# Performance work log

Measured on AMD Instinct MI355X. Metric: run time of the kernel, lower is better.

## Reference

```python
import jax, jax.numpy as jnp
import numpy as np

N, C, H, K, HID = 131072, 256, 8, 128, 1024
SCALE = (C // H) ** -0.5  # 1/sqrt(32)


def layernorm(x, g, b, eps=1e-5):
    mu = jnp.mean(x, axis=-1, keepdims=True)
    var = jnp.var(x, axis=-1, keepdims=True)
    return (x - mu) * jax.lax.rsqrt(var + eps) * g + b


def setup_inputs() -> dict:
    key = jax.random.key(0)
    ks = jax.random.split(key, 8)
    feat = jax.random.normal(ks[0], (N, C), dtype=jnp.float32)
    order = jax.random.permutation(ks[1], N)  # serialized order (gather)
    inverse = jnp.argsort(order)              # scatter back (unpad identity)
    s = 0.02
    return {
        "feat": feat,
        "ln1_g": jnp.ones((C,), jnp.float32), "ln1_b": jnp.zeros((C,), jnp.float32),
        "w_qkv": jax.random.normal(ks[2], (C, 3 * C), jnp.float32) * s,
        "b_qkv": jnp.zeros((3 * C,), jnp.float32),
        "w_proj": jax.random.normal(ks[3], (C, C), jnp.float32) * s,
        "b_proj": jnp.zeros((C,), jnp.float32),
        "ln2_g": jnp.ones((C,), jnp.float32), "ln2_b": jnp.zeros((C,), jnp.float32),
        "w1": jax.random.normal(ks[4], (C, HID), jnp.float32) * s,
        "b1": jnp.zeros((HID,), jnp.float32),
        "w2": jax.random.normal(ks[5], (HID, C), jnp.float32) * s,
        "b2": jnp.zeros((C,), jnp.float32),
        "order": order,
        "inverse": inverse,
    }


def attention(x, w_qkv, b_qkv, w_proj, b_proj, order, inverse):
    D = C // H
    qkv = x @ w_qkv + b_qkv                       # [N, 3C]
    qkv = qkv[order]                              # gather to serialized order
    qkv = qkv.reshape(-1, K, 3, H, D)             # [P, K, 3, H, D]
    q, k, v = jnp.moveaxis(qkv, 2, 0)             # each [P, K, H, D]
    q = jnp.swapaxes(q, 1, 2)                     # [P, H, K, D]
    k = jnp.swapaxes(k, 1, 2)
    v = jnp.swapaxes(v, 1, 2)
    attn = jnp.einsum("phkd,phjd->phkj", q * SCALE, k)  # [P, H, K, K]
    attn = jax.nn.softmax(attn, axis=-1)
    out = jnp.einsum("phkj,phjd->phkd", attn, v)  # [P, H, K, D]
    out = jnp.swapaxes(out, 1, 2).reshape(-1, C)  # [N, C]
    out = out[inverse]                            # scatter back to input order
    return out @ w_proj + b_proj


def reference(feat, ln1_g, ln1_b, w_qkv, b_qkv, w_proj, b_proj,
              ln2_g, ln2_b, w1, b1, w2, b2, order, inverse):
    # pre-norm transformer block: x + attn(ln1(x)); x + mlp(ln2(x))
    x = feat
    x = x + attention(layernorm(x, ln1_g, ln1_b), w_qkv, b_qkv, w_proj, b_proj, order, inverse)
    h = layernorm(x, ln2_g, ln2_b)
    h = jax.nn.gelu(h @ w1 + b1) @ w2 + b2
    return x + h
```

## Files before the change

kernel.cpp:

```cpp
#include <hip/hip_runtime.h>
#include <hip/hip_bf16.h>

typedef __hip_bfloat16 bf16;
typedef __bf16 bf16x8 __attribute__((ext_vector_type(8)));
typedef float f32x4 __attribute__((ext_vector_type(4)));

#define N_TOK 131072
#define C_DIM 256
#define HID_DIM 1024

__device__ __forceinline__ void async_copy16(void* lds, const void* g) {
  __builtin_amdgcn_global_load_lds(
      (const __attribute__((address_space(1))) void*)g,
      (__attribute__((address_space(3))) void*)lds, 16, 0, 0);
}

__device__ __forceinline__ float fast_rcp(float x) {
#if __has_builtin(__builtin_amdgcn_rcpf)
  return __builtin_amdgcn_rcpf(x);
#else
  return 1.f / x;
#endif
}

__device__ __forceinline__ bf16 bf16_rne(float f) {
  unsigned u = __float_as_uint(f);
  u += 0x7FFF + ((u >> 16) & 1);
  unsigned short s = (unsigned short)(u >> 16);
  return *reinterpret_cast<bf16*>(&s);
}

__device__ __forceinline__ float fast_gelu(float x) {
  float t = x * x;
  float u = __builtin_fmaf(0.07135481627f, t, 1.5957691216f);
  float z = x * u;
  float e = __expf(-z);
  return x * fast_rcp(1.f + e);
}

__global__ void ln_bf16_kernel(const float* __restrict__ x,
                               const float* __restrict__ g,
                               const float* __restrict__ b,
                               bf16* __restrict__ out) {
  int row = blockIdx.x * 4 + threadIdx.y;
  int lane = threadIdx.x;
  size_t base = (size_t)row * C_DIM + lane * 4;
  float4 v = *(const float4*)(x + base);
  float s = v.x + v.y + v.z + v.w;
  float s2 = v.x * v.x + v.y * v.y + v.z * v.z + v.w * v.w;
#pragma unroll
  for (int m = 1; m < 64; m <<= 1) { s += __shfl_xor(s, m); s2 += __shfl_xor(s2, m); }
  float mean = s * (1.f / 256.f);
  float var = s2 * (1.f / 256.f) - mean * mean;
  float rstd = rsqrtf(var + 1e-5f);
  float4 gv = *(const float4*)(g + lane * 4);
  float4 bv = *(const float4*)(b + lane * 4);
  union { bf16 h[4]; uint2 u; } pk;
  pk.h[0] = bf16_rne((v.x - mean) * rstd * gv.x + bv.x);
  pk.h[1] = bf16_rne((v.y - mean) * rstd * gv.y + bv.y);
  pk.h[2] = bf16_rne((v.z - mean) * rstd * gv.z + bv.z);
  pk.h[3] = bf16_rne((v.w - mean) * rstd * gv.w + bv.w);
  *(uint2*)(out + base) = pk.u;
}

__global__ void cast_transpose_kernel(const float* __restrict__ in, bf16* __restrict__ out,
                                      int K, int N) {
  int idx = blockIdx.x * 256 + threadIdx.x;
  if (idx >= K * N) return;
  int n = idx / K, k = idx - n * K;
  out[idx] = bf16_rne(in[(size_t)k * N + n]);
}

template <int EPI, int NXT>
__global__ __launch_bounds__(256) void gemm_bt_kernel(
    const bf16* __restrict__ A, const bf16* __restrict__ Bt,
    const float* __restrict__ bias, const float* __restrict__ res,
    void* __restrict__ outp, int K, int ldn) {
  __shared__ bf16 sA[128 * 64];
  __shared__ bf16 sB[128 * 64];
  const int bid = blockIdx.x;
  const int xcd = bid & 7;
  const int j = bid >> 3;
  const int n0 = (j % NXT) * 128;
  const int m0 = ((j / NXT) * 8 + xcd) * 128;
  const int tid = threadIdx.x;
  const int wid = tid >> 6;
  const int lane = tid & 63;
  const int quad = lane >> 4;
  const int l16 = lane & 15;
  const int wm = (wid >> 1) * 64;
  const int wn = (wid & 1) * 64;
  const int srow = tid >> 3;
  const int scol = ((tid & 7) ^ (srow & 7)) * 8;

  const bf16* pA = A + (size_t)(m0 + srow) * K + scol;
  const bf16* pB = Bt + (size_t)(n0 + srow) * K + scol;
  const size_t isStride = (size_t)32 * K;

  f32x4 acc[4][4] = {};

  for (int k0 = 0; k0 < K; k0 += 64) {
#pragma unroll
    for (int is = 0; is < 4; ++is) {
      async_copy16(&sA[is * 2048 + wid * 512], pA + is * isStride);
      async_copy16(&sB[is * 2048 + wid * 512], pB + is * isStride);
    }
    pA += 64;
    pB += 64;
    __syncthreads();
#pragma unroll
    for (int kk = 0; kk < 64; kk += 32) {
      bf16x8 af[4], bfr[4];
#pragma unroll
      for (int i = 0; i < 4; ++i)
        af[i] = *(const bf16x8*)&sA[(wm + i * 16 + l16) * 64 +
                                    ((((kk >> 3) + quad) ^ (l16 & 7)) << 3)];
#pragma unroll
      for (int j2 = 0; j2 < 4; ++j2)
        bfr[j2] = *(const bf16x8*)&sB[(wn + j2 * 16 + l16) * 64 +
                                      ((((kk >> 3) + quad) ^ (l16 & 7)) << 3)];
#pragma unroll
      for (int i = 0; i < 4; ++i)
#pragma unroll
        for (int j2 = 0; j2 < 4; ++j2)
          acc[i][j2] = __builtin_amdgcn_mfma_f32_16x16x32_bf16(af[i], bfr[j2], acc[i][j2], 0, 0, 0);
    }
    __syncthreads();
  }

  float bv[4];
#pragma unroll
  for (int j2 = 0; j2 < 4; ++j2) bv[j2] = bias[n0 + wn + j2 * 16 + l16];
  const int colb = n0 + wn + l16;
#pragma unroll
  for (int i = 0; i < 4; ++i) {
    int rowb = m0 + wm + i * 16 + quad * 4;
#pragma unroll
    for (int r = 0; r < 4; ++r) {
      size_t rowoff = (size_t)(rowb + r) * ldn + colb;
#pragma unroll
      for (int j2 = 0; j2 < 4; ++j2) {
        size_t idx = rowoff + j2 * 16;
        float v = acc[i][j2][r] + bv[j2];
        if constexpr (EPI == 0) {
          ((bf16*)outp)[idx] = bf16_rne(v);
        } else if constexpr (EPI == 1) {
          ((float*)outp)[idx] = v + res[idx];
        } else if constexpr (EPI == 2) {
          ((bf16*)outp)[idx] = bf16_rne(fast_gelu(v));
        } else {
          ((float*)outp)[idx] = v + res[idx];
        }
      }
    }
  }
}

__global__ __launch_bounds__(256) void attn_kernel(
    const bf16* __restrict__ qkv, const int* __restrict__ order,
    bf16* __restrict__ outw) {
  __shared__ bf16 sK[128 * 40];
  __shared__ bf16 sVt[32 * 136];
  __shared__ bf16 sP[128 * 136];
  __shared__ int sOrd[128];
  const int bid = blockIdx.x;
  const int h = (bid >> 3) & 7;
  const int p = ((bid >> 6) << 3) | (bid & 7);
  const int tid = threadIdx.x;
  const int wid = tid >> 6;
  const int lane = tid & 63;
  const int quad = lane >> 4;
  const int l16 = lane & 15;

  if (tid < 128) sOrd[tid] = order[p * 128 + tid];
  __syncthreads();

  {
    int r = tid >> 1;
    int half = (tid & 1) * 16;
    size_t base = (size_t)sOrd[r] * 768 + h * 32;
    uint4 ka = *(const uint4*)&qkv[base + 256 + half];
    uint4 kb = *(const uint4*)&qkv[base + 256 + half + 8];
    *(uint4*)&sK[r * 40 + half] = ka;
    *(uint4*)&sK[r * 40 + half + 8] = kb;
    union { uint4 u[2]; bf16 e[16]; } vv;
    vv.u[0] = *(const uint4*)&qkv[base + 512 + half];
    vv.u[1] = *(const uint4*)&qkv[base + 512 + half + 8];
#pragma unroll
    for (int c = 0; c < 16; ++c) sVt[(half + c) * 136 + r] = vv.e[c];
  }
  __syncthreads();

  bf16x8 qf[2];
#pragma unroll
  for (int t = 0; t < 2; ++t) {
    int r = wid * 32 + t * 16 + l16;
    qf[t] = *(const bf16x8*)&qkv[(size_t)sOrd[r] * 768 + h * 32 + quad * 8];
  }

  const f32x4 zero = {0.f, 0.f, 0.f, 0.f};
  f32x4 s[2][8];
#pragma unroll
  for (int ct = 0; ct < 8; ++ct) {
    bf16x8 kf = *(const bf16x8*)&sK[(ct * 16 + l16) * 40 + quad * 8];
#pragma unroll
    for (int t = 0; t < 2; ++t)
      s[t][ct] = __builtin_amdgcn_mfma_f32_16x16x32_bf16(qf[t], kf, zero, 0, 0, 0);
  }

  const float scale = 0.17677669529663687f;
#pragma unroll
  for (int t = 0; t < 2; ++t) {
#pragma unroll
    for (int r = 0; r < 4; ++r) {
      float mx = -1e30f;
#pragma unroll
      for (int ct = 0; ct < 8; ++ct) mx = fmaxf(mx, s[t][ct][r]);
      mx *= scale;
#pragma unroll
      for (int mk = 1; mk < 16; mk <<= 1) mx = fmaxf(mx, __shfl_xor(mx, mk));
      float sum = 0.f;
#pragma unroll
      for (int ct = 0; ct < 8; ++ct) {
        float e = __expf(scale * s[t][ct][r] - mx);
        s[t][ct][r] = e;
        sum += e;
      }
#pragma unroll
      for (int mk = 1; mk < 16; mk <<= 1) sum += __shfl_xor(sum, mk);
      float inv = fast_rcp(sum);
      int prow = wid * 32 + t * 16 + quad * 4 + r;
#pragma unroll
      for (int ct = 0; ct < 8; ++ct)
        sP[prow * 136 + ct * 16 + l16] = bf16_rne(s[t][ct][r] * inv);
    }
  }
  __syncthreads();

  f32x4 o[2][2] = {};
#pragma unroll
  for (int ks = 0; ks < 4; ++ks) {
    bf16x8 vf[2];
#pragma unroll
    for (int n = 0; n < 2; ++n)
      vf[n] = *(const bf16x8*)&sVt[(n * 16 + l16) * 136 + ks * 32 + quad * 8];
#pragma unroll
    for (int t = 0; t < 2; ++t) {
      bf16x8 pf = *(const bf16x8*)&sP[(wid * 32 + t * 16 + l16) * 136 + ks * 32 + quad * 8];
#pragma unroll
      for (int n = 0; n < 2; ++n)
        o[t][n] = __builtin_amdgcn_mfma_f32_16x16x32_bf16(pf, vf[n], o[t][n], 0, 0, 0);
    }
  }

#pragma unroll
  for (int t = 0; t < 2; ++t) {
    int rowb = wid * 32 + t * 16 + quad * 4;
#pragma unroll
    for (int r = 0; r < 4; ++r) {
      size_t gbase = (size_t)sOrd[rowb + r] * 256 + h * 32;
#pragma unroll
      for (int n = 0; n < 2; ++n)
        outw[gbase + n * 16 + l16] = bf16_rne(o[t][n][r]);
    }
  }
}

extern "C" void kernel_launch(void* const* d_in, const int* in_sizes, int n_in,
                              void* d_out, int out_size, void* d_ws, size_t ws_size,
                              hipStream_t stream) {
  const float* feat   = (const float*)d_in[0];
  const float* ln1_g  = (const float*)d_in[1];
  const float* ln1_b  = (const float*)d_in[2];
  const float* w_qkv  = (const float*)d_in[3];
  const float* b_qkv  = (const float*)d_in[4];
  const float* w_proj = (const float*)d_in[5];
  const float* b_proj = (const float*)d_in[6];
  const float* ln2_g  = (const float*)d_in[7];
  const float* ln2_b  = (const float*)d_in[8];
  const float* w1     = (const float*)d_in[9];
  const float* b1     = (const float*)d_in[10];
  const float* w2     = (const float*)d_in[11];
  const float* b2     = (const float*)d_in[12];
  const int* order    = (const int*)d_in[13];
  float* out = (float*)d_out;

  char* ws = (char*)d_ws;
  size_t off = 0;
  auto take = [&](size_t bytes) {
    char* pp = ws + off;
    off += (bytes + 255) & ~(size_t)255;
    return pp;
  };
  bf16* ln_buf  = (bf16*)take((size_t)N_TOK * 256 * 2);
  bf16* qkv     = (bf16*)take((size_t)N_TOK * 768 * 2);
  bf16* attn_o  = (bf16*)take((size_t)N_TOK * 256 * 2);
  float* xres   = (float*)take((size_t)N_TOK * 256 * 4);
  bf16* wqkvT   = (bf16*)take(768 * 256 * 2);
  bf16* wprojT  = (bf16*)take(256 * 256 * 2);
  bf16* w1T     = (bf16*)take(1024 * 256 * 2);
  bf16* w2T     = (bf16*)take(256 * 1024 * 2);
  bf16* hbuf    = qkv;

  cast_transpose_kernel<<<768, 256, 0, stream>>>(w_qkv, wqkvT, 256, 768);
  cast_transpose_kernel<<<256, 256, 0, stream>>>(w_proj, wprojT, 256, 256);
  cast_transpose_kernel<<<1024, 256, 0, stream>>>(w1, w1T, 256, 1024);
  cast_transpose_kernel<<<1024, 256, 0, stream>>>(w2, w2T, 1024, 256);

  ln_bf16_kernel<<<N_TOK / 4, dim3(64, 4), 0, stream>>>(feat, ln1_g, ln1_b, ln_buf);
  gemm_bt_kernel<0, 6><<<6 * 1024, 256, 0, stream>>>(ln_buf, wqkvT, b_qkv, nullptr, qkv, 256, 768);
  attn_kernel<<<8 * 1024, 256, 0, stream>>>(qkv, order, attn_o);
  gemm_bt_kernel<1, 2><<<2 * 1024, 256, 0, stream>>>(attn_o, wprojT, b_proj, feat, xres, 256, 256);
  ln_bf16_kernel<<<N_TOK / 4, dim3(64, 4), 0, stream>>>(xres, ln2_g, ln2_b, ln_buf);
  gemm_bt_kernel<2, 8><<<8 * 1024, 256, 0, stream>>>(ln_buf, w1T, b1, nullptr, hbuf, 256, 1024);
  gemm_bt_kernel<3, 2><<<2 * 1024, 256, 0, stream>>>(hbuf, w2T, b2, xres, out, 1024, 256);
}
```

Before: 832.6 us.

## Fuse proj with LN2 and MLP up/down GEMMs, restructure QKV GEMM

Replaces the generic tiled GEMM with three specialised kernels. The first is a QKV GEMM that keeps the full-K A tile in registers and streams double-buffered weight chunks. The second fuses the projection GEMM with the residual add and LayerNorm2. The third is a fused MLP kernel that computes each hidden chunk, applies GELU in LDS and immediately accumulates the down projection, so the hidden activation is never written to global memory. This removes several full-size HBM round trips (the fp32 residual, the hidden buffer and the separate LN pass), at the cost of storing the residual in bf16, which lowers precision, and of per-chunk barriers inside the MLP.

```diff
diff --git a/kernel.cpp b/kernel.cpp
--- a/kernel.cpp
+++ b/kernel.cpp
@@ -14,6 +14,8 @@
       (const __attribute__((address_space(1))) void*)g,
       (__attribute__((address_space(3))) void*)lds, 16, 0, 0);
 }
+
+#define PIPE_BARRIER() asm volatile("s_waitcnt vmcnt(0) lgkmcnt(0)\n\ts_barrier" ::: "memory")
 
 __device__ __forceinline__ float fast_rcp(float x) {
 #if __has_builtin(__builtin_amdgcn_rcpf)
@@ -71,87 +73,280 @@
   out[idx] = bf16_rne(in[(size_t)k * N + n]);
 }
 
-template <int EPI, int NXT>
-__global__ __launch_bounds__(256) void gemm_bt_kernel(
+
+__global__ __launch_bounds__(256) void qkv_gemm_kernel(
+    const bf16* __restrict__ A, const bf16* __restrict__ Bt,
+    const float* __restrict__ bias, bf16* __restrict__ out) {
+  __shared__ bf16 sA[64 * 256];
+  __shared__ bf16 sB[2][128 * 32];
+  const int tid = threadIdx.x, wid = tid >> 6, lane = tid & 63;
+  const int quad = lane >> 4, l16 = lane & 15;
+  const int m0 = blockIdx.x * 64;
+
+#pragma unroll
+  for (int s = 0; s < 8; ++s) {
+    int r0 = (s * 4 + wid) * 2;
+    int row = r0 + (lane >> 5), cb = lane & 31;
+    async_copy16(&sA[r0 * 256],
+                 &A[(size_t)(m0 + row) * 256 + ((cb ^ (row & 7)) << 3)]);
+  }
+  {
+#pragma unroll
+    for (int s = 0; s < 2; ++s) {
+      int n0 = s * 64 + wid * 16;
+      int n = n0 + (lane >> 2), cb = lane & 3;
+      async_copy16(&sB[0][n0 * 32],
+                   &Bt[(size_t)n * 256 + ((cb ^ ((n >> 1) & 3)) << 3)]);
+    }
+  }
+
+  bf16x8 af[2][8];
+  f32x4 acc[2][4];
+
+  for (int i = 0; i < 48; ++i) {
+    const int nc = i >> 3, kc = i & 7;
+    PIPE_BARRIER();
+    if (i == 0) {
+#pragma unroll
+      for (int i2 = 0; i2 < 2; ++i2)
+#pragma unroll
+        for (int ks = 0; ks < 8; ++ks) {
+          int row = (wid & 1) * 32 + i2 * 16 + l16;
+          af[i2][ks] = *(const bf16x8*)&sA[row * 256 + (((ks * 4 + quad) ^ (row & 7)) << 3)];
+        }
+    }
+    if (i + 1 < 48) {
+      const int nc2 = (i + 1) >> 3, kc2 = (i + 1) & 7, nb = (i + 1) & 1;
+#pragma unroll
+      for (int s = 0; s < 2; ++s) {
+        int n0 = s * 64 + wid * 16;
+        int n = n0 + (lane >> 2), cb = lane & 3;
+        async_copy16(&sB[nb][n0 * 32],
+                     &Bt[(size_t)(nc2 * 128 + n) * 256 + kc2 * 32 + ((cb ^ ((n >> 1) & 3)) << 3)]);
+      }
+    }
+    if (kc == 0) {
+#pragma unroll
+      for (int i2 = 0; i2 < 2; ++i2)
+#pragma unroll
+        for (int j = 0; j < 4; ++j) acc[i2][j] = (f32x4){0.f, 0.f, 0.f, 0.f};
+    }
+    const bf16* bs = sB[i & 1];
+#pragma unroll
+    for (int j = 0; j < 4; ++j) {
+      int n = (wid >> 1) * 64 + j * 16 + l16;
+      bf16x8 bfr = *(const bf16x8*)&bs[n * 32 + ((quad ^ ((l16 >> 1) & 3)) << 3)];
+#pragma unroll
+      for (int i2 = 0; i2 < 2; ++i2)
+        acc[i2][j] = __builtin_amdgcn_mfma_f32_16x16x32_bf16(af[i2][kc], bfr, acc[i2][j], 0, 0, 0);
+    }
+    if (kc == 7) {
+#pragma unroll
+      for (int i2 = 0; i2 < 2; ++i2) {
+        int rowb = m0 + (wid & 1) * 32 + i2 * 16 + quad * 4;
+#pragma unroll
+        for (int j = 0; j < 4; ++j) {
+          int col = nc * 128 + (wid >> 1) * 64 + j * 16 + l16;
+          float bv = bias[col];
+#pragma unroll
+          for (int r = 0; r < 4; ++r)
+            out[(size_t)(rowb + r) * 768 + col] = bf16_rne(acc[i2][j][r] + bv);
+        }
+      }
+    }
+  }
+}
+
+__global__ __launch_bounds__(256) void proj_ln2_kernel(
     const bf16* __restrict__ A, const bf16* __restrict__ Bt,
     const float* __restrict__ bias, const float* __restrict__ res,
-    void* __restrict__ outp, int K, int ldn) {
-  __shared__ bf16 sA[128 * 64];
-  __shared__ bf16 sB[128 * 64];
-  const int bid = blockIdx.x;
-  const int xcd = bid & 7;
-  const int j = bid >> 3;
-  const int n0 = (j % NXT) * 128;
-  const int m0 = ((j / NXT) * 8 + xcd) * 128;
-  const int tid = threadIdx.x;
-  const int wid = tid >> 6;
-  const int lane = tid & 63;
-  const int quad = lane >> 4;
-  const int l16 = lane & 15;
-  const int wm = (wid >> 1) * 64;
-  const int wn = (wid & 1) * 64;
-  const int srow = tid >> 3;
-  const int scol = ((tid & 7) ^ (srow & 7)) * 8;
-
-  const bf16* pA = A + (size_t)(m0 + srow) * K + scol;
-  const bf16* pB = Bt + (size_t)(n0 + srow) * K + scol;
-  const size_t isStride = (size_t)32 * K;
-
-  f32x4 acc[4][4] = {};
-
-  for (int k0 = 0; k0 < K; k0 += 64) {
-#pragma unroll
-    for (int is = 0; is < 4; ++is) {
-      async_copy16(&sA[is * 2048 + wid * 512], pA + is * isStride);
-      async_copy16(&sB[is * 2048 + wid * 512], pB + is * isStride);
-    }
-    pA += 64;
-    pB += 64;
+    const float* __restrict__ g, const float* __restrict__ b,
+    bf16* __restrict__ xres, bf16* __restrict__ ln2out) {
+  __shared__ bf16 sA[64 * 256];
+  __shared__ bf16 sB[2][256 * 32];
+  const int tid = threadIdx.x, wid = tid >> 6, lane = tid & 63;
+  const int quad = lane >> 4, l16 = lane & 15;
+  const int m0 = blockIdx.x * 64;
+
+#pragma unroll
+  for (int s = 0; s < 8; ++s) {
+    int r0 = (s * 4 + wid) * 2;
+    int row = r0 + (lane >> 5), cb = lane & 31;
+    async_copy16(&sA[r0 * 256],
+                 &A[(size_t)(m0 + row) * 256 + ((cb ^ (row & 7)) << 3)]);
+  }
+#pragma unroll
+  for (int s = 0; s < 4; ++s) {
+    int n0 = s * 64 + wid * 16;
+    int n = n0 + (lane >> 2), cb = lane & 3;
+    async_copy16(&sB[0][n0 * 32],
+                 &Bt[(size_t)n * 256 + ((cb ^ ((n >> 1) & 3)) << 3)]);
+  }
+
+  bf16x8 af[8];
+  f32x4 acc[16] = {};
+
+  for (int kc = 0; kc < 8; ++kc) {
+    PIPE_BARRIER();
+    if (kc == 0) {
+#pragma unroll
+      for (int ks = 0; ks < 8; ++ks) {
+        int row = wid * 16 + l16;
+        af[ks] = *(const bf16x8*)&sA[row * 256 + (((ks * 4 + quad) ^ (row & 7)) << 3)];
+      }
+    }
+    if (kc < 7) {
+      const int nb = (kc + 1) & 1;
+#pragma unroll
+      for (int s = 0; s < 4; ++s) {
+        int n0 = s * 64 + wid * 16;
+        int n = n0 + (lane >> 2), cb = lane & 3;
+        async_copy16(&sB[nb][n0 * 32],
+                     &Bt[(size_t)n * 256 + (kc + 1) * 32 + ((cb ^ ((n >> 1) & 3)) << 3)]);
+      }
+    }
+    const bf16* bs = sB[kc & 1];
+#pragma unroll
+    for (int j = 0; j < 16; ++j) {
+      int n = j * 16 + l16;
+      bf16x8 bfr = *(const bf16x8*)&bs[n * 32 + ((quad ^ ((l16 >> 1) & 3)) << 3)];
+      acc[j] = __builtin_amdgcn_mfma_f32_16x16x32_bf16(af[kc], bfr, acc[j], 0, 0, 0);
+    }
+  }
+
+  const int rowq = m0 + wid * 16 + quad * 4;
+  float s1[4] = {0.f, 0.f, 0.f, 0.f}, s2[4] = {0.f, 0.f, 0.f, 0.f};
+#pragma unroll
+  for (int j = 0; j < 16; ++j) {
+    int col = j * 16 + l16;
+    float bv = bias[col];
+#pragma unroll
+    for (int r = 0; r < 4; ++r) {
+      float v = acc[j][r] + bv + res[(size_t)(rowq + r) * 256 + col];
+      acc[j][r] = v;
+      s1[r] += v;
+      s2[r] += v * v;
+    }
+  }
+#pragma unroll
+  for (int r = 0; r < 4; ++r)
+#pragma unroll
+    for (int mk = 1; mk < 16; mk <<= 1) {
+      s1[r] += __shfl_xor(s1[r], mk);
+      s2[r] += __shfl_xor(s2[r], mk);
+    }
+  float mean[4], rstd[4];
+#pragma unroll
+  for (int r = 0; r < 4; ++r) {
+    mean[r] = s1[r] * (1.f / 256.f);
+    float var = s2[r] * (1.f / 256.f) - mean[r] * mean[r];
+    rstd[r] = rsqrtf(var + 1e-5f);
+  }
+#pragma unroll
+  for (int j = 0; j < 16; ++j) {
+    int col = j * 16 + l16;
+    float gv = g[col], bl = b[col];
+#pragma unroll
+    for (int r = 0; r < 4; ++r) {
+      size_t idx = (size_t)(rowq + r) * 256 + col;
+      float v = acc[j][r];
+      xres[idx] = bf16_rne(v);
+      ln2out[idx] = bf16_rne((v - mean[r]) * rstd[r] * gv + bl);
+    }
+  }
+}
+
+__global__ __launch_bounds__(512) void mlp_fused_kernel(
+    const bf16* __restrict__ A, const bf16* __restrict__ W1t,
+    const float* __restrict__ b1, const bf16* __restrict__ W2t,
+    const float* __restrict__ b2, const bf16* __restrict__ res,
+    float* __restrict__ out) {
+  __shared__ bf16 sA[128 * 256];
+  __shared__ bf16 sW1[32 * 256];
+  __shared__ bf16 sW2[256 * 32];
+  __shared__ bf16 sH[128 * 40];
+  const int tid = threadIdx.x, w = tid >> 6, lane = tid & 63;
+  const int quad = lane >> 4, l16 = lane & 15;
+  const int m0 = blockIdx.x * 128;
+  const int q1 = (w & 3) * 32;
+  const int nh = (w >> 2) * 16;
+
+#pragma unroll
+  for (int s = 0; s < 8; ++s) {
+    int r0 = (s * 8 + w) * 2;
+    int row = r0 + (lane >> 5), cb = lane & 31;
+    async_copy16(&sA[r0 * 256],
+                 &A[(size_t)(m0 + row) * 256 + ((cb ^ (row & 7)) << 3)]);
+  }
+
+  bf16x8 af1[2][8];
+  f32x4 acc2[16] = {};
+
+  for (int c = 0; c < 32; ++c) {
     __syncthreads();
 #pragma unroll
-    for (int kk = 0; kk < 64; kk += 32) {
-      bf16x8 af[4], bfr[4];
-#pragma unroll
-      for (int i = 0; i < 4; ++i)
-        af[i] = *(const bf16x8*)&sA[(wm + i * 16 + l16) * 64 +
-                                    ((((kk >> 3) + quad) ^ (l16 & 7)) << 3)];
-#pragma unroll
-      for (int j2 = 0; j2 < 4; ++j2)
-        bfr[j2] = *(const bf16x8*)&sB[(wn + j2 * 16 + l16) * 64 +
-                                      ((((kk >> 3) + quad) ^ (l16 & 7)) << 3)];
-#pragma unroll
-      for (int i = 0; i < 4; ++i)
-#pragma unroll
-        for (int j2 = 0; j2 < 4; ++j2)
-          acc[i][j2] = __builtin_amdgcn_mfma_f32_16x16x32_bf16(af[i], bfr[j2], acc[i][j2], 0, 0, 0);
+    for (int s = 0; s < 2; ++s) {
+      int r0 = s * 16 + w * 2;
+      int row = r0 + (lane >> 5), cb = lane & 31;
+      async_copy16(&sW1[r0 * 256],
+                   &W1t[(size_t)(c * 32 + row) * 256 + ((cb ^ (row & 7)) << 3)]);
+    }
+#pragma unroll
+    for (int s = 0; s < 2; ++s) {
+      int n0 = s * 128 + w * 16;
+      int n = n0 + (lane >> 2), cb = lane & 3;
+      async_copy16(&sW2[n0 * 32],
+                   &W2t[(size_t)n * 1024 + c * 32 + ((cb ^ ((n >> 1) & 3)) << 3)]);
     }
     __syncthreads();
-  }
-
-  float bv[4];
-#pragma unroll
-  for (int j2 = 0; j2 < 4; ++j2) bv[j2] = bias[n0 + wn + j2 * 16 + l16];
-  const int colb = n0 + wn + l16;
-#pragma unroll
-  for (int i = 0; i < 4; ++i) {
-    int rowb = m0 + wm + i * 16 + quad * 4;
+    if (c == 0) {
+#pragma unroll
+      for (int i = 0; i < 2; ++i)
+#pragma unroll
+        for (int ks = 0; ks < 8; ++ks) {
+          int row = q1 + i * 16 + l16;
+          af1[i][ks] = *(const bf16x8*)&sA[row * 256 + (((ks * 4 + quad) ^ (row & 7)) << 3)];
+        }
+    }
+    f32x4 a1[2] = {};
+#pragma unroll
+    for (int ks = 0; ks < 8; ++ks) {
+      int n = nh + l16;
+      bf16x8 b1f = *(const bf16x8*)&sW1[n * 256 + (((ks * 4 + quad) ^ (n & 7)) << 3)];
+#pragma unroll
+      for (int i = 0; i < 2; ++i)
+        a1[i] = __builtin_amdgcn_mfma_f32_16x16x32_bf16(af1[i][ks], b1f, a1[i], 0, 0, 0);
+    }
+    float bb = b1[c * 32 + nh + l16];
+#pragma unroll
+    for (int i = 0; i < 2; ++i) {
+      int rowb = q1 + i * 16 + quad * 4;
+#pragma unroll
+      for (int r = 0; r < 4; ++r)
+        sH[(rowb + r) * 40 + nh + l16] = bf16_rne(fast_gelu(a1[i][r] + bb));
+    }
+    __syncthreads();
+    {
+      int m = w * 16 + l16;
+      bf16x8 a2f = *(const bf16x8*)&sH[m * 40 + quad * 8];
+#pragma unroll
+      for (int j = 0; j < 16; ++j) {
+        int n = j * 16 + l16;
+        bf16x8 b2f = *(const bf16x8*)&sW2[n * 32 + ((quad ^ ((l16 >> 1) & 3)) << 3)];
+        acc2[j] = __builtin_amdgcn_mfma_f32_16x16x32_bf16(a2f, b2f, acc2[j], 0, 0, 0);
+      }
+    }
+  }
+
+  const int rowq = m0 + w * 16 + quad * 4;
+#pragma unroll
+  for (int j = 0; j < 16; ++j) {
+    int col = j * 16 + l16;
+    float bv = b2[col];
 #pragma unroll
     for (int r = 0; r < 4; ++r) {
-      size_t rowoff = (size_t)(rowb + r) * ldn + colb;
-#pragma unroll
-      for (int j2 = 0; j2 < 4; ++j2) {
-        size_t idx = rowoff + j2 * 16;
-        float v = acc[i][j2][r] + bv[j2];
-        if constexpr (EPI == 0) {
-          ((bf16*)outp)[idx] = bf16_rne(v);
-        } else if constexpr (EPI == 1) {
-          ((float*)outp)[idx] = v + res[idx];
-        } else if constexpr (EPI == 2) {
-          ((bf16*)outp)[idx] = bf16_rne(fast_gelu(v));
-        } else {
-          ((float*)outp)[idx] = v + res[idx];
-        }
-      }
+      size_t idx = (size_t)(rowq + r) * 256 + col;
+      out[idx] = acc2[j][r] + bv + __bfloat162float(res[idx]);
     }
   }
 }
@@ -295,12 +490,11 @@
   bf16* ln_buf  = (bf16*)take((size_t)N_TOK * 256 * 2);
   bf16* qkv     = (bf16*)take((size_t)N_TOK * 768 * 2);
   bf16* attn_o  = (bf16*)take((size_t)N_TOK * 256 * 2);
-  float* xres   = (float*)take((size_t)N_TOK * 256 * 4);
+  bf16* xresb   = (bf16*)take((size_t)N_TOK * 256 * 2);
   bf16* wqkvT   = (bf16*)take(768 * 256 * 2);
   bf16* wprojT  = (bf16*)take(256 * 256 * 2);
   bf16* w1T     = (bf16*)take(1024 * 256 * 2);
   bf16* w2T     = (bf16*)take(256 * 1024 * 2);
-  bf16* hbuf    = qkv;
 
   cast_transpose_kernel<<<768, 256, 0, stream>>>(w_qkv, wqkvT, 256, 768);
   cast_transpose_kernel<<<256, 256, 0, stream>>>(w_proj, wprojT, 256, 256);
@@ -308,10 +502,9 @@
   cast_transpose_kernel<<<1024, 256, 0, stream>>>(w2, w2T, 1024, 256);
 
   ln_bf16_kernel<<<N_TOK / 4, dim3(64, 4), 0, stream>>>(feat, ln1_g, ln1_b, ln_buf);
-  gemm_bt_kernel<0, 6><<<6 * 1024, 256, 0, stream>>>(ln_buf, wqkvT, b_qkv, nullptr, qkv, 256, 768);
+  qkv_gemm_kernel<<<N_TOK / 64, 256, 0, stream>>>(ln_buf, wqkvT, b_qkv, qkv);
   attn_kernel<<<8 * 1024, 256, 0, stream>>>(qkv, order, attn_o);
-  gemm_bt_kernel<1, 2><<<2 * 1024, 256, 0, stream>>>(attn_o, wprojT, b_proj, feat, xres, 256, 256);
-  ln_bf16_kernel<<<N_TOK / 4, dim3(64, 4), 0, stream>>>(xres, ln2_g, ln2_b, ln_buf);
-  gemm_bt_kernel<2, 8><<<8 * 1024, 256, 0, stream>>>(ln_buf, w1T, b1, nullptr, hbuf, 256, 1024);
-  gemm_bt_kernel<3, 2><<<2 * 1024, 256, 0, stream>>>(hbuf, w2T, b2, xres, out, 1024, 256);
-}
+  proj_ln2_kernel<<<N_TOK / 64, 256, 0, stream>>>(attn_o, wprojT, b_proj, feat,
+                                                  ln2_g, ln2_b, xresb, ln_buf);
+  mlp_fused_kernel<<<N_TOK / 128, 512, 0, stream>>>(ln_buf, w1T, b1, w2T, b2, xresb, out);
+}
```

Result: slower. 1.101 ms (+32.3%).
